# Kernel optimization log

Measured on AMD Instinct MI355X. Metric: run time of the kernel, lower is better.

## Reference

```python
import jax, jax.numpy as jnp
import numpy as np

D = 768
H = 12
MLP = 3072
EPS = 1e-5


def _layernorm(x, g, b):
    mu = jnp.mean(x, axis=-1, keepdims=True)
    var = jnp.var(x, axis=-1, keepdims=True)
    return (x - mu) * jax.lax.rsqrt(var + EPS) * g + b


def setup_inputs() -> dict:
    key = jax.random.key(0)
    ks = jax.random.split(key, 16)
    s = 0.02
    inp = {
        "x": jax.random.normal(ks[0], (8, 1024, D), dtype=jnp.float32),
        "ln1_g": jnp.ones((D,), jnp.float32),
        "ln1_b": jnp.zeros((D,), jnp.float32),
        "Wq": jax.random.normal(ks[1], (D, D), jnp.float32) * s,
        "bq": jnp.zeros((D,), jnp.float32),
        "Wk": jax.random.normal(ks[2], (D, D), jnp.float32) * s,
        "bk": jnp.zeros((D,), jnp.float32),
        "Wv": jax.random.normal(ks[3], (D, D), jnp.float32) * s,
        "bv": jnp.zeros((D,), jnp.float32),
        "Wo": jax.random.normal(ks[4], (D, D), jnp.float32) * s,
        "bo": jnp.zeros((D,), jnp.float32),
        "ln2_g": jnp.ones((D,), jnp.float32),
        "ln2_b": jnp.zeros((D,), jnp.float32),
        "W1": jax.random.normal(ks[5], (D, MLP), jnp.float32) * s,
        "b1": jnp.zeros((MLP,), jnp.float32),
        "W2": jax.random.normal(ks[6], (MLP, D), jnp.float32) * s,
        "b2": jnp.zeros((D,), jnp.float32),
    }
    return inp


def reference(x, ln1_g, ln1_b, Wq, bq, Wk, bk, Wv, bv, Wo, bo, ln2_g, ln2_b, W1, b1, W2, b2):
    b, n, d = x.shape
    dh = d // H
    scale = 1.0 / jnp.sqrt(jnp.float32(d))  # NOTE: sqrt(input_dim), per source

    h = _layernorm(x, ln1_g, ln1_b)
    q = (h @ Wq + bq).reshape(b, n, H, dh).transpose(0, 2, 1, 3)  # bhnf
    k = (h @ Wk + bk).reshape(b, n, H, dh).transpose(0, 2, 1, 3)
    v = (h @ Wv + bv).reshape(b, n, H, dh).transpose(0, 2, 1, 3)

    score = jax.nn.softmax(jnp.einsum('bhif,bhjf->bhij', q, k) * scale, axis=-1)
    attn = jnp.einsum('bhij,bhjf->bihf', score, v).reshape(b, n, d)
    out = attn @ Wo + bo + x  # residual (dropout p=0)

    h2 = _layernorm(out, ln2_g, ln2_b)
    mlp = jax.nn.gelu(jax.nn.gelu(h2 @ W1 + b1, approximate=False) @ W2 + b2, approximate=False)
    return mlp + out
```

## Files before the change

kernel.cpp:

```cpp
#include <hip/hip_runtime.h>
#include <hip/hip_bf16.h>
#include <math.h>

typedef __bf16 bf16x8 __attribute__((ext_vector_type(8)));
typedef float f32x4 __attribute__((ext_vector_type(4)));

#define DD 768
#define HH 12
#define MLPD 3072
#define QSCALE 0.036084391824351615f

__device__ __forceinline__ float gelu_fast(float x) {
    float y = 1.5957691216057308f * x + 0.07135481283154893f * x * x * x;
    return x * __builtin_amdgcn_rcpf(1.0f + __expf(-y));
}

__device__ __forceinline__ void gload16(const void* g, void* l) {
    __builtin_amdgcn_global_load_lds(
        (const __attribute__((address_space(1))) unsigned int*)g,
        (__attribute__((address_space(3))) unsigned int*)l, 16, 0, 0);
}

__global__ __launch_bounds__(256) void wtrans_all(
    const float* __restrict__ Wq, const float* __restrict__ Wk,
    const float* __restrict__ Wv, const float* __restrict__ Wo,
    const float* __restrict__ W1, const float* __restrict__ W2,
    __bf16* __restrict__ wqkv, __bf16* __restrict__ wo,
    __bf16* __restrict__ w1, __bf16* __restrict__ w2) {
    __shared__ float tile[64][65];
    int b = blockIdx.x;
    const float* W; __bf16* Wt; int K, N, tk, tn;
    if (b < 432) {
        int wsel = b / 144, r = b - wsel * 144;
        W = wsel == 0 ? Wq : (wsel == 1 ? Wk : Wv);
        Wt = wqkv + (size_t)wsel * 768 * 768;
        K = 768; N = 768; tk = r % 12; tn = r / 12;
    } else if (b < 576) {
        int r = b - 432; W = Wo; Wt = wo; K = 768; N = 768; tk = r % 12; tn = r / 12;
    } else if (b < 1152) {
        int r = b - 576; W = W1; Wt = w1; K = 768; N = 3072; tk = r % 12; tn = r / 12;
    } else {
        int r = b - 1152; W = W2; Wt = w2; K = 3072; N = 768; tk = r % 48; tn = r / 48;
    }
    int k0 = tk * 64, n0 = tn * 64;
    int t = threadIdx.x;
    int tr = t >> 6, tc = t & 63;
#pragma unroll
    for (int i = 0; i < 16; ++i) {
        int row = i * 4 + tr;
        tile[row][tc] = W[(size_t)(k0 + row) * N + n0 + tc];
    }
    __syncthreads();
#pragma unroll
    for (int i = 0; i < 16; ++i) {
        int row = i * 4 + tr;
        Wt[(size_t)(n0 + row) * K + k0 + tc] = (__bf16)tile[tc][row];
    }
}

__global__ __launch_bounds__(64) void ln_kernel(const float* __restrict__ X,
                                                const float* __restrict__ g,
                                                const float* __restrict__ b,
                                                __bf16* __restrict__ O) {
    int row = blockIdx.x;
    int lane = threadIdx.x;
    const float* xr = X + (size_t)row * DD;
    float4 v[3];
    float s = 0.f, ss = 0.f;
#pragma unroll
    for (int i = 0; i < 3; ++i) {
        v[i] = *reinterpret_cast<const float4*>(&xr[(i * 64 + lane) * 4]);
        s += v[i].x + v[i].y + v[i].z + v[i].w;
        ss += v[i].x * v[i].x + v[i].y * v[i].y + v[i].z * v[i].z + v[i].w * v[i].w;
    }
#pragma unroll
    for (int m = 1; m < 64; m <<= 1) {
        s += __shfl_xor(s, m);
        ss += __shfl_xor(ss, m);
    }
    float mu = s * (1.0f / DD);
    float rstd = rsqrtf(ss * (1.0f / DD) - mu * mu + 1e-5f);
#pragma unroll
    for (int i = 0; i < 3; ++i) {
        int c = (i * 64 + lane) * 4;
        float4 gv = *reinterpret_cast<const float4*>(&g[c]);
        float4 bv = *reinterpret_cast<const float4*>(&b[c]);
        union { __bf16 h[4]; uint2 u; } o;
        o.h[0] = (__bf16)((v[i].x - mu) * rstd * gv.x + bv.x);
        o.h[1] = (__bf16)((v[i].y - mu) * rstd * gv.y + bv.y);
        o.h[2] = (__bf16)((v[i].z - mu) * rstd * gv.z + bv.z);
        o.h[3] = (__bf16)((v[i].w - mu) * rstd * gv.w + bv.w);
        *reinterpret_cast<uint2*>(&O[(size_t)row * DD + c]) = o.u;
    }
}

template <int EPI>
__global__ __launch_bounds__(256, 2) void gemm_pl(
    const __bf16* __restrict__ A, const __bf16* __restrict__ Bt,
    const float* __restrict__ b0, const float* __restrict__ b1, const float* __restrict__ b2,
    void* __restrict__ o0, void* __restrict__ o1, void* __restrict__ o2,
    const float* __restrict__ resid, int M, int N, int K) {
    extern __shared__ __bf16 lds[];
    __bf16* As = lds;
    __bf16* Bs = lds + 16384;
    const int t = threadIdx.x;
    const int w = t >> 6, lane = t & 63;
    const int wm = w >> 1, wn = w & 1;
    const int lr = lane & 15, lg = lane >> 4;
    const int m0 = blockIdx.x * 128, n0 = blockIdx.y * 128;
    const int lrow8 = lane >> 3;
    const int cSwz = ((lane & 7) ^ lrow8) * 8;

    const __bf16* aSrc = A + (size_t)(m0 + w * 32 + lrow8) * K + cSwz;
    const __bf16* bSrc = Bt + (size_t)(n0 + w * 32 + lrow8) * K + cSwz;
    const int ldsW = w * 32 * 64;

    const int nt = K >> 6;
    f32x4 acc[4][4] = {};

    auto stage = [&](int T) {
        const int buf = (T & 1) * 8192;
#pragma unroll
        for (int c = 0; c < 4; ++c)
            gload16(aSrc + (size_t)(c * 8) * K + T * 64, &As[buf + ldsW + c * 8 * 64]);
#pragma unroll
        for (int c = 0; c < 4; ++c)
            gload16(bSrc + (size_t)(c * 8) * K + T * 64, &Bs[buf + ldsW + c * 8 * 64]);
    };

    stage(0);
    for (int T = 0; T < nt; ++T) {
        if (T + 1 < nt) {
            stage(T + 1);
            asm volatile("s_waitcnt vmcnt(8)" ::: "memory");
        } else {
            asm volatile("s_waitcnt vmcnt(0)" ::: "memory");
        }
        __builtin_amdgcn_s_barrier();
        const int buf = (T & 1) * 8192;
#pragma unroll
        for (int kg = 0; kg < 2; ++kg) {
            bf16x8 af[4], bfr[4];
#pragma unroll
            for (int i = 0; i < 4; ++i)
                af[i] = *reinterpret_cast<const bf16x8*>(
                    &As[buf + (wm * 64 + i * 16 + lr) * 64 + (((kg << 2) | lg) ^ (lr & 7)) * 8]);
#pragma unroll
            for (int j = 0; j < 4; ++j)
                bfr[j] = *reinterpret_cast<const bf16x8*>(
                    &Bs[buf + (wn * 64 + j * 16 + lr) * 64 + (((kg << 2) | lg) ^ (lr & 7)) * 8]);
            asm volatile("s_waitcnt lgkmcnt(0)" ::: "memory");
            __builtin_amdgcn_sched_barrier(0);
            __builtin_amdgcn_s_setprio(1);
#pragma unroll
            for (int i = 0; i < 4; ++i)
#pragma unroll
                for (int j = 0; j < 4; ++j)
                    acc[i][j] = __builtin_amdgcn_mfma_f32_16x16x32_bf16(bfr[j], af[i], acc[i][j], 0, 0, 0);
            __builtin_amdgcn_s_setprio(0);
        }
        __builtin_amdgcn_s_barrier();
    }

#pragma unroll
    for (int i = 0; i < 4; ++i) {
        const int m = m0 + wm * 64 + i * 16 + lr;
        const int bI = m >> 10, ntok = m & 1023;
#pragma unroll
        for (int j = 0; j < 4; ++j) {
            const int n = n0 + wn * 64 + j * 16 + lg * 4;
            if (EPI == 0) {
                const int wid = n / 768;
                const int cc0 = n - wid * 768;
                const int hh = cc0 >> 6, f0 = cc0 & 63;
                const float* bsel = (wid == 0 ? b0 : (wid == 1 ? b1 : b2));
                const float4 bv = *reinterpret_cast<const float4*>(&bsel[cc0]);
                const float v0 = acc[i][j][0] + bv.x, v1 = acc[i][j][1] + bv.y;
                const float v2 = acc[i][j][2] + bv.z, v3 = acc[i][j][3] + bv.w;
                if (wid == 0) {
                    union { __bf16 h[4]; uint2 u; } pk;
                    pk.h[0] = (__bf16)(v0 * QSCALE); pk.h[1] = (__bf16)(v1 * QSCALE);
                    pk.h[2] = (__bf16)(v2 * QSCALE); pk.h[3] = (__bf16)(v3 * QSCALE);
                    *reinterpret_cast<uint2*>(
                        &((__bf16*)o0)[((((size_t)(bI * HH + hh) << 10) + ntok) << 6) + f0]) = pk.u;
                } else if (wid == 1) {
                    union { __bf16 h[4]; uint2 u; } pk;
                    pk.h[0] = (__bf16)v0; pk.h[1] = (__bf16)v1;
                    pk.h[2] = (__bf16)v2; pk.h[3] = (__bf16)v3;
                    *reinterpret_cast<uint2*>(
                        &((__bf16*)o1)[((((size_t)(bI * HH + hh) << 10) + ntok) << 6) + f0]) = pk.u;
                } else {
                    __bf16* vb = (__bf16*)o2;
                    size_t base = ((size_t)(bI * HH + hh) * 64 + f0) << 10;
                    vb[base + ntok] = (__bf16)v0;
                    vb[base + (1 << 10) + ntok] = (__bf16)v1;
                    vb[base + (2 << 10) + ntok] = (__bf16)v2;
                    vb[base + (3 << 10) + ntok] = (__bf16)v3;
                }
            } else if (EPI == 3) {
                const float4 bv = *reinterpret_cast<const float4*>(&b0[n]);
                union { __bf16 h[4]; uint2 u; } pk;
                pk.h[0] = (__bf16)gelu_fast(acc[i][j][0] + bv.x);
                pk.h[1] = (__bf16)gelu_fast(acc[i][j][1] + bv.y);
                pk.h[2] = (__bf16)gelu_fast(acc[i][j][2] + bv.z);
                pk.h[3] = (__bf16)gelu_fast(acc[i][j][3] + bv.w);
                *reinterpret_cast<uint2*>(&((__bf16*)o0)[(size_t)m * MLPD + n]) = pk.u;
            } else {
                const float4 bv = *reinterpret_cast<const float4*>(&b0[n]);
                const float v0 = acc[i][j][0] + bv.x, v1 = acc[i][j][1] + bv.y;
                const float v2 = acc[i][j][2] + bv.z, v3 = acc[i][j][3] + bv.w;
                const float4 rv = *reinterpret_cast<const float4*>(&resid[(size_t)m * DD + n]);
                if (EPI == 2) {
                    float4 ov = {v0 + rv.x, v1 + rv.y, v2 + rv.z, v3 + rv.w};
                    *reinterpret_cast<float4*>(&((float*)o0)[(size_t)m * DD + n]) = ov;
                } else {
                    float4 ov = {gelu_fast(v0) + rv.x, gelu_fast(v1) + rv.y,
                                 gelu_fast(v2) + rv.z, gelu_fast(v3) + rv.w};
                    *reinterpret_cast<float4*>(&((float*)o0)[(size_t)m * DD + n]) = ov;
                }
            }
        }
    }
}

__global__ __launch_bounds__(512, 6) void attn_kernel(
    const __bf16* __restrict__ Q, const __bf16* __restrict__ Kg,
    const __bf16* __restrict__ Vt, __bf16* __restrict__ Aout) {
    __shared__ char KsB[2][64 * 128];
    __shared__ char VsB[2][64 * 128];
    __shared__ char PsB[8][16 * 128];
    const int id = blockIdx.x;
    const int swz = (id & 7) * 96 + (id >> 3);
    const int bh = swz >> 3, qt = swz & 7;
    const int t = threadIdx.x, w = t >> 6, lane = t & 63;
    const int lr = lane & 15, lg = lane >> 4;
    const size_t bhN = (size_t)bh << 10;
    const int q0 = qt * 128;

    bf16x8 qf[2];
#pragma unroll
    for (int kg = 0; kg < 2; ++kg)
        qf[kg] = *reinterpret_cast<const bf16x8*>(&Q[(bhN + q0 + w * 16 + lr) * 64 + kg * 32 + lg * 8]);

    const int srow = t >> 3;
    const int sc = ((t & 7) ^ (srow & 7)) * 16;
    const char* kbase = (const char*)Kg + bhN * 128;
    const char* vbase = (const char*)Vt + ((size_t)bh << 17);
    const int wlds = w * 1024;

    f32x4 oacc[4] = {};
    float lsum[4] = {0.f, 0.f, 0.f, 0.f};

    gload16(kbase + (size_t)srow * 128 + sc, KsB[0] + wlds);
    gload16(vbase + (size_t)srow * 2048 + sc, VsB[0] + wlds);

    for (int kt = 0; kt < 16; ++kt) {
        const int buf = kt & 1;
        if (kt < 15) {
            gload16(kbase + (size_t)((kt + 1) * 64 + srow) * 128 + sc, KsB[buf ^ 1] + wlds);
            gload16(vbase + (size_t)srow * 2048 + (kt + 1) * 128 + sc, VsB[buf ^ 1] + wlds);
            asm volatile("s_waitcnt vmcnt(2)" ::: "memory");
        } else {
            asm volatile("s_waitcnt vmcnt(0)" ::: "memory");
        }
        __builtin_amdgcn_s_barrier();

        f32x4 s[4] = {};
        __builtin_amdgcn_s_setprio(1);
#pragma unroll
        for (int kg = 0; kg < 2; ++kg) {
#pragma unroll
            for (int j = 0; j < 4; ++j) {
                int row = j * 16 + lr;
                bf16x8 kf = *reinterpret_cast<const bf16x8*>(
                    KsB[buf] + ((row * 128 + kg * 64 + lg * 16) ^ ((row & 7) << 4)));
                s[j] = __builtin_amdgcn_mfma_f32_16x16x32_bf16(qf[kg], kf, s[j], 0, 0, 0);
            }
        }
        __builtin_amdgcn_s_setprio(0);
#pragma unroll
        for (int r = 0; r < 4; ++r) {
            int prow = lg * 4 + r;
#pragma unroll
            for (int j = 0; j < 4; ++j) {
                float pv = __expf(s[j][r]);
                lsum[r] += pv;
                *reinterpret_cast<__bf16*>(
                    PsB[w] + ((prow * 128 + (j * 16 + lr) * 2) ^ ((prow & 7) << 4))) = (__bf16)pv;
            }
        }
        __builtin_amdgcn_s_setprio(1);
#pragma unroll
        for (int kg = 0; kg < 2; ++kg) {
            bf16x8 pf = *reinterpret_cast<const bf16x8*>(
                PsB[w] + ((lr * 128 + kg * 64 + lg * 16) ^ ((lr & 7) << 4)));
#pragma unroll
            for (int j = 0; j < 4; ++j) {
                int row = j * 16 + lr;
                bf16x8 vf = *reinterpret_cast<const bf16x8*>(
                    VsB[buf] + ((row * 128 + kg * 64 + lg * 16) ^ ((row & 7) << 4)));
                oacc[j] = __builtin_amdgcn_mfma_f32_16x16x32_bf16(pf, vf, oacc[j], 0, 0, 0);
            }
        }
        __builtin_amdgcn_s_setprio(0);
        __builtin_amdgcn_s_barrier();
    }

#pragma unroll
    for (int r = 0; r < 4; ++r)
#pragma unroll
        for (int m = 1; m < 16; m <<= 1) lsum[r] += __shfl_xor(lsum[r], m);

    const int bI = bh / HH, hh = bh % HH;
#pragma unroll
    for (int r = 0; r < 4; ++r) {
        float inv = 1.0f / lsum[r];
        int qrow = q0 + w * 16 + lg * 4 + r;
        size_t base = ((size_t)(bI << 10) + qrow) * DD + hh * 64;
#pragma unroll
        for (int j = 0; j < 4; ++j)
            Aout[base + j * 16 + lr] = (__bf16)(oacc[j][r] * inv);
    }
}

extern "C" void kernel_launch(void* const* d_in, const int* in_sizes, int n_in,
                              void* d_out, int out_size, void* d_ws, size_t ws_size,
                              hipStream_t stream) {
    const float* x     = (const float*)d_in[0];
    const float* ln1_g = (const float*)d_in[1];
    const float* ln1_b = (const float*)d_in[2];
    const float* Wq    = (const float*)d_in[3];
    const float* bq    = (const float*)d_in[4];
    const float* Wk    = (const float*)d_in[5];
    const float* bk    = (const float*)d_in[6];
    const float* Wv    = (const float*)d_in[7];
    const float* bv    = (const float*)d_in[8];
    const float* Wo    = (const float*)d_in[9];
    const float* bo    = (const float*)d_in[10];
    const float* ln2_g = (const float*)d_in[11];
    const float* ln2_b = (const float*)d_in[12];
    const float* W1    = (const float*)d_in[13];
    const float* b1    = (const float*)d_in[14];
    const float* W2    = (const float*)d_in[15];
    const float* b2    = (const float*)d_in[16];

    char* p = (char*)d_ws;
    auto alloc = [&](size_t bytes) { char* r = p; p += bytes; return r; };
    __bf16* wqkv_t = (__bf16*)alloc((size_t)2304 * 768 * 2);
    __bf16* wo_t   = (__bf16*)alloc((size_t)768 * 768 * 2);
    __bf16* w1_t   = (__bf16*)alloc((size_t)3072 * 768 * 2);
    __bf16* w2_t   = (__bf16*)alloc((size_t)768 * 3072 * 2);
    __bf16* h      = (__bf16*)alloc((size_t)8192 * 768 * 2);
    float*  outb   = (float*) alloc((size_t)8192 * 768 * 4);
    __bf16* q      = (__bf16*)alloc((size_t)8192 * 768 * 2);
    __bf16* kb     = (__bf16*)alloc((size_t)8192 * 768 * 2);
    __bf16* vt     = (__bf16*)alloc((size_t)8192 * 768 * 2);
    __bf16* attn   = (__bf16*)alloc((size_t)8192 * 768 * 2);
    __bf16* mid    = q;

    const int LDSP = 65536;
    hipFuncSetAttribute(reinterpret_cast<const void*>(gemm_pl<0>),
                        hipFuncAttributeMaxDynamicSharedMemorySize, LDSP);
    hipFuncSetAttribute(reinterpret_cast<const void*>(gemm_pl<2>),
                        hipFuncAttributeMaxDynamicSharedMemorySize, LDSP);
    hipFuncSetAttribute(reinterpret_cast<const void*>(gemm_pl<3>),
                        hipFuncAttributeMaxDynamicSharedMemorySize, LDSP);
    hipFuncSetAttribute(reinterpret_cast<const void*>(gemm_pl<4>),
                        hipFuncAttributeMaxDynamicSharedMemorySize, LDSP);

    wtrans_all<<<1728, 256, 0, stream>>>(Wq, Wk, Wv, Wo, W1, W2, wqkv_t, wo_t, w1_t, w2_t);

    ln_kernel<<<8192, 64, 0, stream>>>(x, ln1_g, ln1_b, h);
    gemm_pl<0><<<dim3(64, 18), 256, LDSP, stream>>>(h, wqkv_t, bq, bk, bv, q, kb, vt,
                                                    nullptr, 8192, 2304, 768);
    attn_kernel<<<768, 512, 0, stream>>>(q, kb, vt, attn);
    gemm_pl<2><<<dim3(64, 6), 256, LDSP, stream>>>(attn, wo_t, bo, nullptr, nullptr, outb,
                                                   nullptr, nullptr, x, 8192, 768, 768);
    ln_kernel<<<8192, 64, 0, stream>>>(outb, ln2_g, ln2_b, h);
    gemm_pl<3><<<dim3(64, 24), 256, LDSP, stream>>>(h, w1_t, b1, nullptr, nullptr, mid,
                                                    nullptr, nullptr, nullptr, 8192, 3072, 768);
    gemm_pl<4><<<dim3(64, 6), 256, LDSP, stream>>>(mid, w2_t, b2, nullptr, nullptr, (float*)d_out,
                                                   nullptr, nullptr, outb, 8192, 768, 3072);
}
```

Measured before the change: 239.6 us.

## Merge weight transpose with first layernorm and interleave softmax with PV MFMAs

```diff
diff --git a/kernel.cpp b/kernel.cpp
--- a/kernel.cpp
+++ b/kernel.cpp
@@ -21,50 +21,10 @@
         (__attribute__((address_space(3))) unsigned int*)l, 16, 0, 0);
 }
 
-__global__ __launch_bounds__(256) void wtrans_all(
-    const float* __restrict__ Wq, const float* __restrict__ Wk,
-    const float* __restrict__ Wv, const float* __restrict__ Wo,
-    const float* __restrict__ W1, const float* __restrict__ W2,
-    __bf16* __restrict__ wqkv, __bf16* __restrict__ wo,
-    __bf16* __restrict__ w1, __bf16* __restrict__ w2) {
-    __shared__ float tile[64][65];
-    int b = blockIdx.x;
-    const float* W; __bf16* Wt; int K, N, tk, tn;
-    if (b < 432) {
-        int wsel = b / 144, r = b - wsel * 144;
-        W = wsel == 0 ? Wq : (wsel == 1 ? Wk : Wv);
-        Wt = wqkv + (size_t)wsel * 768 * 768;
-        K = 768; N = 768; tk = r % 12; tn = r / 12;
-    } else if (b < 576) {
-        int r = b - 432; W = Wo; Wt = wo; K = 768; N = 768; tk = r % 12; tn = r / 12;
-    } else if (b < 1152) {
-        int r = b - 576; W = W1; Wt = w1; K = 768; N = 3072; tk = r % 12; tn = r / 12;
-    } else {
-        int r = b - 1152; W = W2; Wt = w2; K = 3072; N = 768; tk = r % 48; tn = r / 48;
-    }
-    int k0 = tk * 64, n0 = tn * 64;
-    int t = threadIdx.x;
-    int tr = t >> 6, tc = t & 63;
-#pragma unroll
-    for (int i = 0; i < 16; ++i) {
-        int row = i * 4 + tr;
-        tile[row][tc] = W[(size_t)(k0 + row) * N + n0 + tc];
-    }
-    __syncthreads();
-#pragma unroll
-    for (int i = 0; i < 16; ++i) {
-        int row = i * 4 + tr;
-        Wt[(size_t)(n0 + row) * K + k0 + tc] = (__bf16)tile[tc][row];
-    }
-}
-
-__global__ __launch_bounds__(64) void ln_kernel(const float* __restrict__ X,
-                                                const float* __restrict__ g,
-                                                const float* __restrict__ b,
-                                                __bf16* __restrict__ O) {
-    int row = blockIdx.x;
-    int lane = threadIdx.x;
-    const float* xr = X + (size_t)row * DD;
+__device__ __forceinline__ void ln_row(const float* __restrict__ xr,
+                                       const float* __restrict__ g,
+                                       const float* __restrict__ b,
+                                       __bf16* __restrict__ orow, int lane) {
     float4 v[3];
     float s = 0.f, ss = 0.f;
 #pragma unroll
@@ -90,7 +50,59 @@
         o.h[1] = (__bf16)((v[i].y - mu) * rstd * gv.y + bv.y);
         o.h[2] = (__bf16)((v[i].z - mu) * rstd * gv.z + bv.z);
         o.h[3] = (__bf16)((v[i].w - mu) * rstd * gv.w + bv.w);
-        *reinterpret_cast<uint2*>(&O[(size_t)row * DD + c]) = o.u;
+        *reinterpret_cast<uint2*>(&orow[c]) = o.u;
+    }
+}
+
+__global__ __launch_bounds__(256) void ln_kernel(const float* __restrict__ X,
+                                                 const float* __restrict__ g,
+                                                 const float* __restrict__ b,
+                                                 __bf16* __restrict__ O) {
+    int row = blockIdx.x * 4 + (threadIdx.x >> 6);
+    ln_row(X + (size_t)row * DD, g, b, O + (size_t)row * DD, threadIdx.x & 63);
+}
+
+__global__ __launch_bounds__(256) void prep_kernel(
+    const float* __restrict__ Wq, const float* __restrict__ Wk,
+    const float* __restrict__ Wv, const float* __restrict__ Wo,
+    const float* __restrict__ W1, const float* __restrict__ W2,
+    __bf16* __restrict__ wqkv, __bf16* __restrict__ wo,
+    __bf16* __restrict__ w1, __bf16* __restrict__ w2,
+    const float* __restrict__ x, const float* __restrict__ ln1_g,
+    const float* __restrict__ ln1_b, __bf16* __restrict__ h) {
+    __shared__ float tile[64][65];
+    int blk = blockIdx.x;
+    if (blk >= 1728) {
+        int row = (blk - 1728) * 4 + (threadIdx.x >> 6);
+        ln_row(x + (size_t)row * DD, ln1_g, ln1_b, h + (size_t)row * DD, threadIdx.x & 63);
+        return;
+    }
+    const float* W; __bf16* Wt; int K, N, tk, tn;
+    if (blk < 432) {
+        int wsel = blk / 144, r = blk - wsel * 144;
+        W = wsel == 0 ? Wq : (wsel == 1 ? Wk : Wv);
+        Wt = wqkv + (size_t)wsel * 768 * 768;
+        K = 768; N = 768; tk = r % 12; tn = r / 12;
+    } else if (blk < 576) {
+        int r = blk - 432; W = Wo; Wt = wo; K = 768; N = 768; tk = r % 12; tn = r / 12;
+    } else if (blk < 1152) {
+        int r = blk - 576; W = W1; Wt = w1; K = 768; N = 3072; tk = r % 12; tn = r / 12;
+    } else {
+        int r = blk - 1152; W = W2; Wt = w2; K = 3072; N = 768; tk = r % 48; tn = r / 48;
+    }
+    int k0 = tk * 64, n0 = tn * 64;
+    int t = threadIdx.x;
+    int tr = t >> 6, tc = t & 63;
+#pragma unroll
+    for (int i = 0; i < 16; ++i) {
+        int row = i * 4 + tr;
+        tile[row][tc] = W[(size_t)(k0 + row) * N + n0 + tc];
+    }
+    __syncthreads();
+#pragma unroll
+    for (int i = 0; i < 16; ++i) {
+        int row = i * 4 + tr;
+        Wt[(size_t)(n0 + row) * K + k0 + tc] = (__bf16)tile[tc][row];
     }
 }
 
@@ -278,31 +290,47 @@
             }
         }
         __builtin_amdgcn_s_setprio(0);
+
 #pragma unroll
         for (int r = 0; r < 4; ++r) {
             int prow = lg * 4 + r;
 #pragma unroll
-            for (int j = 0; j < 4; ++j) {
+            for (int j = 0; j < 2; ++j) {
                 float pv = __expf(s[j][r]);
                 lsum[r] += pv;
                 *reinterpret_cast<__bf16*>(
                     PsB[w] + ((prow * 128 + (j * 16 + lr) * 2) ^ ((prow & 7) << 4))) = (__bf16)pv;
             }
         }
-        __builtin_amdgcn_s_setprio(1);
-#pragma unroll
-        for (int kg = 0; kg < 2; ++kg) {
-            bf16x8 pf = *reinterpret_cast<const bf16x8*>(
-                PsB[w] + ((lr * 128 + kg * 64 + lg * 16) ^ ((lr & 7) << 4)));
-#pragma unroll
-            for (int j = 0; j < 4; ++j) {
-                int row = j * 16 + lr;
-                bf16x8 vf = *reinterpret_cast<const bf16x8*>(
-                    VsB[buf] + ((row * 128 + kg * 64 + lg * 16) ^ ((row & 7) << 4)));
-                oacc[j] = __builtin_amdgcn_mfma_f32_16x16x32_bf16(pf, vf, oacc[j], 0, 0, 0);
+        bf16x8 pf0 = *reinterpret_cast<const bf16x8*>(
+            PsB[w] + ((lr * 128 + 0 * 64 + lg * 16) ^ ((lr & 7) << 4)));
+#pragma unroll
+        for (int r = 0; r < 4; ++r) {
+            int prow = lg * 4 + r;
+#pragma unroll
+            for (int j = 2; j < 4; ++j) {
+                float pv = __expf(s[j][r]);
+                lsum[r] += pv;
+                *reinterpret_cast<__bf16*>(
+                    PsB[w] + ((prow * 128 + (j * 16 + lr) * 2) ^ ((prow & 7) << 4))) = (__bf16)pv;
             }
         }
-        __builtin_amdgcn_s_setprio(0);
+#pragma unroll
+        for (int j = 0; j < 4; ++j) {
+            int row = j * 16 + lr;
+            bf16x8 vf = *reinterpret_cast<const bf16x8*>(
+                VsB[buf] + ((row * 128 + 0 * 64 + lg * 16) ^ ((row & 7) << 4)));
+            oacc[j] = __builtin_amdgcn_mfma_f32_16x16x32_bf16(pf0, vf, oacc[j], 0, 0, 0);
+        }
+        bf16x8 pf1 = *reinterpret_cast<const bf16x8*>(
+            PsB[w] + ((lr * 128 + 1 * 64 + lg * 16) ^ ((lr & 7) << 4)));
+#pragma unroll
+        for (int j = 0; j < 4; ++j) {
+            int row = j * 16 + lr;
+            bf16x8 vf = *reinterpret_cast<const bf16x8*>(
+                VsB[buf] + ((row * 128 + 1 * 64 + lg * 16) ^ ((row & 7) << 4)));
+            oacc[j] = __builtin_amdgcn_mfma_f32_16x16x32_bf16(pf1, vf, oacc[j], 0, 0, 0);
+        }
         __builtin_amdgcn_s_barrier();
     }
 
@@ -368,15 +396,15 @@
     hipFuncSetAttribute(reinterpret_cast<const void*>(gemm_pl<4>),
                         hipFuncAttributeMaxDynamicSharedMemorySize, LDSP);
 
-    wtrans_all<<<1728, 256, 0, stream>>>(Wq, Wk, Wv, Wo, W1, W2, wqkv_t, wo_t, w1_t, w2_t);
-
-    ln_kernel<<<8192, 64, 0, stream>>>(x, ln1_g, ln1_b, h);
+    prep_kernel<<<3776, 256, 0, stream>>>(Wq, Wk, Wv, Wo, W1, W2,
+                                          wqkv_t, wo_t, w1_t, w2_t,
+                                          x, ln1_g, ln1_b, h);
     gemm_pl<0><<<dim3(64, 18), 256, LDSP, stream>>>(h, wqkv_t, bq, bk, bv, q, kb, vt,
                                                     nullptr, 8192, 2304, 768);
     attn_kernel<<<768, 512, 0, stream>>>(q, kb, vt, attn);
     gemm_pl<2><<<dim3(64, 6), 256, LDSP, stream>>>(attn, wo_t, bo, nullptr, nullptr, outb,
                                                    nullptr, nullptr, x, 8192, 768, 768);
-    ln_kernel<<<8192, 64, 0, stream>>>(outb, ln2_g, ln2_b, h);
+    ln_kernel<<<2048, 256, 0, stream>>>(outb, ln2_g, ln2_b, h);
     gemm_pl<3><<<dim3(64, 24), 256, LDSP, stream>>>(h, w1_t, b1, nullptr, nullptr, mid,
                                                     nullptr, nullptr, nullptr, 8192, 3072, 768);
     gemm_pl<4><<<dim3(64, 6), 256, LDSP, stream>>>(mid, w2_t, b2, nullptr, nullptr, (float*)d_out,
```

Measured after the change: 238.3 us. Within noise of the previous version (-0.5%).
